# Performance work log

Hardware: AMD Instinct MI355X
Metric: run time of the kernel (lower is better)

## Reference

```python
import jax, jax.numpy as jnp
import numpy as np

N_FFT = 1024
HOP = 256
F_BINS = N_FFT // 2 + 1  # 513


def _make_dft_kernel():
    # torch.hann_window(N) is periodic: 0.5*(1 - cos(2*pi*k/N))
    window = 0.5 * (1.0 - np.cos(2.0 * np.pi * np.arange(N_FFT) / N_FFT))
    # rfft of identity, transposed -> (F, n_fft), then apply window along time axis
    dftm = np.fft.rfft(np.eye(N_FFT)).T * window[None, :]  # complex (F, n_fft)
    # view_as_real + rearrange 'f n ri -> (ri f) n': real block first, imag block second
    kernel = np.concatenate([dftm.real, dftm.imag], axis=0)  # (2F, n_fft)
    return jnp.asarray(kernel, dtype=jnp.float32)


def setup_inputs() -> dict:
    key = jax.random.key(0)
    signal = jax.random.normal(key, (16, 262144), dtype=jnp.float32)
    kernel = _make_dft_kernel()  # (1026, 1024) fixed windowed-DFT matrix (buffer)
    return {"signal": signal, "kernel": kernel}


def reference(signal, kernel):
    # center=True: reflect-pad by n_fft//2 on both sides
    pad = N_FFT // 2
    x = jnp.pad(signal, ((0, 0), (pad, pad)), mode="reflect")  # (B, L)
    B, L = x.shape
    n_frames = (L - N_FFT) // HOP + 1
    # im2col framing: (n_frames, n_fft) gather indices
    idx = jnp.arange(n_frames)[:, None] * HOP + jnp.arange(N_FFT)[None, :]
    frames = x[:, idx]  # (B, n_frames, n_fft)
    # conv1d as GEMM: (B, 2F, n_frames)
    out = jnp.einsum("btn,cn->bct", frames, kernel)
    # rearrange '(ri f) n -> f n ri' with ri outer
    out = out.reshape(B, 2, F_BINS, n_frames)
    return jnp.transpose(out, (0, 2, 3, 1))  # (B, F, n_frames, 2)
```

## Files before the change

### kernel.cpp

```cpp
#include <hip/hip_runtime.h>
#include <hip/hip_bf16.h>
#include <cstdint>


#define HOP 256
#define NFFT 1024
#define FB 513
#define NT 1025
#define NBATCH 16
#define MCH 1026
#define MP2 1280
#define SIGLEN 262144
#define SIGP 263168
#define BM 256
#define BN 128
#define BK 64
#define NKT 16
#define SLOT_BYTES 49152
#define LDS_BYTES (3 * SLOT_BYTES)

typedef __attribute__((ext_vector_type(8))) short short8;
typedef __attribute__((ext_vector_type(4))) float f32x4;
typedef unsigned int u32;

__device__ __forceinline__ unsigned short f2bf(float f) {
  u32 u = __float_as_uint(f);
  u = (u + 0x7FFFu + ((u >> 16) & 1u)) >> 16;
  return (unsigned short)u;
}
__device__ __forceinline__ float bf2f(unsigned short s) {
  return __uint_as_float(((u32)s) << 16);
}

__global__ __launch_bounds__(256) void prep_A(const float* __restrict__ kern,
                                              unsigned short* __restrict__ A) {
  size_t i8 = ((size_t)blockIdx.x * 256 + threadIdx.x) * 8;
  int row = (int)(i8 >> 10);
  int col = (int)(i8 & 1023);
  short8 v = {0, 0, 0, 0, 0, 0, 0, 0};
  if (row < MCH) {
    int f = row >> 1, ri = row & 1;
    int src_row = ri * FB + f;
    const float* s = kern + ((size_t)src_row << 10) + col;
#pragma unroll
    for (int e = 0; e < 8; ++e) v[e] = (short)f2bf(s[e]);
  }
  *(short8*)(A + i8) = v;
}

__global__ __launch_bounds__(256) void prep_S(const float* __restrict__ sig,
                                              unsigned short* __restrict__ S) {
  size_t i8 = ((size_t)blockIdx.x * 256 + threadIdx.x) * 8;
  int b = (int)(i8 / SIGP);
  int i = (int)(i8 - (size_t)b * SIGP);
  const float* sb = sig + (size_t)b * SIGLEN;
  short8 v;
#pragma unroll
  for (int e = 0; e < 8; ++e) {
    int j = i + e - 512;
    j = (j < 0) ? -j : j;
    j = (j >= SIGLEN) ? (2 * SIGLEN - 2 - j) : j;
    v[e] = (short)f2bf(sb[j]);
  }
  *(short8*)(S + i8) = v;
}

__device__ __forceinline__ void async16(void* lds, const void* g) {
  __builtin_amdgcn_global_load_lds(
      (const __attribute__((address_space(1))) u32*)g,
      (__attribute__((address_space(3))) u32*)lds, 16, 0, 0);
}

__global__ __launch_bounds__(512, 2) void stft_mm(const unsigned short* __restrict__ A,
                                                  const unsigned short* __restrict__ S,
                                                  float* __restrict__ out) {
  extern __shared__ char smem[];

  const int tid = threadIdx.x;
  const int lane = tid & 63;
  const int wid = tid >> 6;
  const int wr = wid >> 1;
  const int wc = wid & 1;
  const int lr = lane & 15;
  const int g16 = lane >> 4;

  const int bid = blockIdx.x;
  const int wg = (bid & 7) * 64 + (bid >> 3);
  const int mt = wg & 3;
  const int r2 = wg >> 2;
  const int nt = r2 & 7;
  const int b  = r2 >> 3;

  const int c0 = mt * BM;
  const int t0 = nt * BN;

  const char* Ab = (const char*)A;
  const char* Sb = (const char*)(S + (size_t)b * SIGP);

#define STAGE_TILE(kt, s)                                                      \
  {                                                                            \
    char* As_ = smem + (s) * SLOT_BYTES;                                       \
    char* Bs_ = As_ + 32768;                                                   \
    _Pragma("unroll") for (int j = 0; j < 4; ++j) {                            \
      const int G0 = j * 512 + wid * 64;                                       \
      u32 p = (u32)(G0 + lane) * 16u;                                          \
      u32 q = p ^ (((p >> 7) & 7u) << 4);                                      \
      const char* src = Ab + ((size_t)(c0 + (int)(q >> 7)) << 11)              \
                           + (kt) * 128 + (int)(q & 127u);                     \
      async16(As_ + (size_t)G0 * 16u, src);                                    \
    }                                                                          \
    _Pragma("unroll") for (int j = 0; j < 2; ++j) {                            \
      const int G0 = j * 512 + wid * 64;                                       \
      u32 p = (u32)(G0 + lane) * 16u;                                          \
      u32 q = p ^ (((p >> 7) & 7u) << 4);                                      \
      const char* src = Sb + ((size_t)(t0 + (int)(q >> 7)) << 9)               \
                           + (kt) * 128 + (int)(q & 127u);                     \
      async16(Bs_ + (size_t)G0 * 16u, src);                                    \
    }                                                                          \
  }

  STAGE_TILE(0, 0)
  STAGE_TILE(1, 1)
  asm volatile("s_waitcnt vmcnt(6)" ::: "memory");
  __builtin_amdgcn_s_barrier();
  asm volatile("" ::: "memory");

  u32 qa[4], qb[4];
#pragma unroll
  for (int mi = 0; mi < 4; ++mi) qa[mi] = (u32)((wr * 64 + mi * 16 + lr) * 128 + g16 * 16);
#pragma unroll
  for (int ni = 0; ni < 4; ++ni) qb[ni] = (u32)((wc * 64 + ni * 16 + lr) * 128 + g16 * 16);

  f32x4 acc[4][4] = {};

#pragma unroll
  for (int k = 0; k < NKT; ++k) {
    const char* As = smem + (k % 3) * SLOT_BYTES;
    const char* Bs = As + 32768;
    short8 af[2][4], bfv[2][4];
#pragma unroll
    for (int h = 0; h < 2; ++h) {
#pragma unroll
      for (int mi = 0; mi < 4; ++mi) {
        u32 q = qa[mi] + (u32)(h * 64);
        u32 p = q ^ (((q >> 7) & 7u) << 4);
        af[h][mi] = *(const short8*)(As + p);
      }
#pragma unroll
      for (int ni = 0; ni < 4; ++ni) {
        u32 q = qb[ni] + (u32)(h * 64);
        u32 p = q ^ (((q >> 7) & 7u) << 4);
        bfv[h][ni] = *(const short8*)(Bs + p);
      }
    }
    if (k + 2 < NKT) STAGE_TILE(k + 2, (k + 2) % 3)
#pragma unroll
    for (int h = 0; h < 2; ++h)
#pragma unroll
      for (int mi = 0; mi < 4; ++mi)
#pragma unroll
        for (int ni = 0; ni < 4; ++ni)
          acc[mi][ni] = __builtin_amdgcn_mfma_f32_16x16x32_bf16(
              af[h][mi], bfv[h][ni], acc[mi][ni], 0, 0, 0);
    if (k <= NKT - 3)      asm volatile("s_waitcnt vmcnt(6)" ::: "memory");
    else                   asm volatile("s_waitcnt vmcnt(0)" ::: "memory");
    __builtin_amdgcn_s_barrier();
    asm volatile("" ::: "memory");
  }
#undef STAGE_TILE

#pragma unroll
  for (int mi = 0; mi < 4; ++mi) {
    const int cb = c0 + wr * 64 + mi * 16 + g16 * 4;
    const int f0 = cb >> 1;
#pragma unroll
    for (int ni = 0; ni < 4; ++ni) {
      const int t = t0 + wc * 64 + ni * 16 + lr;
      *(float2*)(out + ((((size_t)b * FB + f0) * NT + t) << 1)) =
          make_float2(acc[mi][ni][0], acc[mi][ni][1]);
      *(float2*)(out + ((((size_t)b * FB + f0 + 1) * NT + t) << 1)) =
          make_float2(acc[mi][ni][2], acc[mi][ni][3]);
    }
  }
}

__global__ __launch_bounds__(256) void stft_edge(const unsigned short* __restrict__ A,
                                                 const unsigned short* __restrict__ S,
                                                 float* __restrict__ out) {
  const int wv = blockIdx.x * 4 + (threadIdx.x >> 6);
  const int lane = threadIdx.x & 63;
  int b, f, t;
  if (wv < NBATCH * NT) {
    b = wv / NT; t = wv - b * NT; f = FB - 1;
  } else {
    int u = wv - NBATCH * NT;
    b = u / FB; f = u - b * FB; t = NT - 1;
  }
  const unsigned short* w  = S + (size_t)b * SIGP + (size_t)t * HOP + lane * 16;
  const unsigned short* r0 = A + ((size_t)(2 * f) << 10) + lane * 16;
  const unsigned short* r1 = r0 + 1024;
  short8 wv0 = *(const short8*)w,  wv1 = *(const short8*)(w + 8);
  short8 a0  = *(const short8*)r0, a1  = *(const short8*)(r0 + 8);
  short8 b0  = *(const short8*)r1, b1  = *(const short8*)(r1 + 8);
  float d0 = 0.f, d1 = 0.f;
#pragma unroll
  for (int e = 0; e < 8; ++e) {
    float x0 = bf2f((unsigned short)wv0[e]), x1 = bf2f((unsigned short)wv1[e]);
    d0 += bf2f((unsigned short)a0[e]) * x0 + bf2f((unsigned short)a1[e]) * x1;
    d1 += bf2f((unsigned short)b0[e]) * x0 + bf2f((unsigned short)b1[e]) * x1;
  }
#pragma unroll
  for (int m = 32; m; m >>= 1) {
    d0 += __shfl_xor(d0, m);
    d1 += __shfl_xor(d1, m);
  }
  if (lane == 0)
    *(float2*)(out + ((((size_t)b * FB + f) * NT + t) << 1)) = make_float2(d0, d1);
}

extern "C" void kernel_launch(void* const* d_in, const int* in_sizes, int n_in,
                              void* d_out, int out_size, void* d_ws, size_t ws_size,
                              hipStream_t stream) {
  const float* sig = (const float*)d_in[0];
  const float* kern = (const float*)d_in[1];
  float* out = (float*)d_out;

  unsigned short* wsA = (unsigned short*)d_ws;
  unsigned short* wsS = wsA + (size_t)MP2 * NFFT;

  (void)hipFuncSetAttribute((const void*)stft_mm,
                            hipFuncAttributeMaxDynamicSharedMemorySize, LDS_BYTES);

  prep_A<<<dim3(MP2 * NFFT / 8 / 256), 256, 0, stream>>>(kern, wsA);
  prep_S<<<dim3(NBATCH * SIGP / 8 / 256), 256, 0, stream>>>(sig, wsS);
  stft_mm<<<dim3(4 * 8 * NBATCH), 512, LDS_BYTES, stream>>>(wsA, wsS, out);
  stft_edge<<<dim3((NBATCH * NT + NBATCH * FB) / 4), 256, 0, stream>>>(wsA, wsS, out);
}
```

Before: 64.97 us.

## Halve K tile to 32 and switch to double-buffered static LDS pipeline

The GEMM K-step drops from 64 to 32 and the three-slot, two-ahead async pipeline becomes a two-slot, one-ahead one held in static shared memory (48KB instead of 144KB). Launch bounds now request 4 blocks per CU instead of 2, and the swizzle is changed to match the 64-byte rows. The intent is higher occupancy and less LDS pressure. In exchange there are twice as many barriers per tile, less prefetch depth, and a full __syncthreads that waits on all outstanding loads. Only 512 blocks are launched, so there may be too few blocks to use the extra occupancy.

```diff
diff --git a/kernel.cpp b/kernel.cpp
--- a/kernel.cpp
+++ b/kernel.cpp
@@ -14,10 +14,11 @@
 #define SIGP 263168
 #define BM 256
 #define BN 128
-#define BK 64
-#define NKT 16
-#define SLOT_BYTES 49152
-#define LDS_BYTES (3 * SLOT_BYTES)
+#define BK 32
+#define NKT 32
+#define A_BYTES 16384
+#define B_BYTES 8192
+#define SLOT_BYTES (A_BYTES + B_BYTES)
 
 typedef __attribute__((ext_vector_type(8))) short short8;
 typedef __attribute__((ext_vector_type(4))) float f32x4;
@@ -71,10 +72,10 @@
       (__attribute__((address_space(3))) u32*)lds, 16, 0, 0);
 }
 
-__global__ __launch_bounds__(512, 2) void stft_mm(const unsigned short* __restrict__ A,
+__global__ __launch_bounds__(512, 4) void stft_mm(const unsigned short* __restrict__ A,
                                                   const unsigned short* __restrict__ S,
                                                   float* __restrict__ out) {
-  extern __shared__ char smem[];
+  __shared__ __align__(16) char smem[2][SLOT_BYTES];
 
   const int tid = threadIdx.x;
   const int lane = tid & 63;
@@ -99,73 +100,64 @@
 
 #define STAGE_TILE(kt, s)                                                      \
   {                                                                            \
-    char* As_ = smem + (s) * SLOT_BYTES;                                       \
-    char* Bs_ = As_ + 32768;                                                   \
-    _Pragma("unroll") for (int j = 0; j < 4; ++j) {                            \
-      const int G0 = j * 512 + wid * 64;                                       \
-      u32 p = (u32)(G0 + lane) * 16u;                                          \
-      u32 q = p ^ (((p >> 7) & 7u) << 4);                                      \
-      const char* src = Ab + ((size_t)(c0 + (int)(q >> 7)) << 11)              \
-                           + (kt) * 128 + (int)(q & 127u);                     \
-      async16(As_ + (size_t)G0 * 16u, src);                                    \
-    }                                                                          \
+    char* As_ = &smem[s][0];                                                   \
+    char* Bs_ = &smem[s][A_BYTES];                                             \
     _Pragma("unroll") for (int j = 0; j < 2; ++j) {                            \
       const int G0 = j * 512 + wid * 64;                                       \
       u32 p = (u32)(G0 + lane) * 16u;                                          \
-      u32 q = p ^ (((p >> 7) & 7u) << 4);                                      \
-      const char* src = Sb + ((size_t)(t0 + (int)(q >> 7)) << 9)               \
-                           + (kt) * 128 + (int)(q & 127u);                     \
+      u32 q = p ^ (((p >> 7) & 3u) << 4);                                      \
+      const char* src = Ab + ((size_t)(c0 + (int)(q >> 6)) << 11)              \
+                           + (kt) * 64 + (int)(q & 63u);                       \
+      async16(As_ + (size_t)G0 * 16u, src);                                    \
+    }                                                                          \
+    {                                                                          \
+      const int G0 = wid * 64;                                                 \
+      u32 p = (u32)(G0 + lane) * 16u;                                          \
+      u32 q = p ^ (((p >> 7) & 3u) << 4);                                      \
+      const char* src = Sb + ((size_t)(t0 + (int)(q >> 6)) << 9)               \
+                           + (kt) * 64 + (int)(q & 63u);                       \
       async16(Bs_ + (size_t)G0 * 16u, src);                                    \
     }                                                                          \
   }
 
   STAGE_TILE(0, 0)
-  STAGE_TILE(1, 1)
-  asm volatile("s_waitcnt vmcnt(6)" ::: "memory");
-  __builtin_amdgcn_s_barrier();
-  asm volatile("" ::: "memory");
-
-  u32 qa[4], qb[4];
-#pragma unroll
-  for (int mi = 0; mi < 4; ++mi) qa[mi] = (u32)((wr * 64 + mi * 16 + lr) * 128 + g16 * 16);
-#pragma unroll
-  for (int ni = 0; ni < 4; ++ni) qb[ni] = (u32)((wc * 64 + ni * 16 + lr) * 128 + g16 * 16);
+  __syncthreads();
+
+  u32 pa[4], pb[4];
+#pragma unroll
+  for (int mi = 0; mi < 4; ++mi) {
+    u32 q = (u32)((wr * 64 + mi * 16 + lr) * 64 + g16 * 16);
+    pa[mi] = q ^ (((q >> 7) & 3u) << 4);
+  }
+#pragma unroll
+  for (int ni = 0; ni < 4; ++ni) {
+    u32 q = (u32)((wc * 64 + ni * 16 + lr) * 64 + g16 * 16);
+    pb[ni] = q ^ (((q >> 7) & 3u) << 4);
+  }
 
   f32x4 acc[4][4] = {};
 
 #pragma unroll
   for (int k = 0; k < NKT; ++k) {
-    const char* As = smem + (k % 3) * SLOT_BYTES;
-    const char* Bs = As + 32768;
-    short8 af[2][4], bfv[2][4];
-#pragma unroll
-    for (int h = 0; h < 2; ++h) {
-#pragma unroll
-      for (int mi = 0; mi < 4; ++mi) {
-        u32 q = qa[mi] + (u32)(h * 64);
-        u32 p = q ^ (((q >> 7) & 7u) << 4);
-        af[h][mi] = *(const short8*)(As + p);
-      }
-#pragma unroll
-      for (int ni = 0; ni < 4; ++ni) {
-        u32 q = qb[ni] + (u32)(h * 64);
-        u32 p = q ^ (((q >> 7) & 7u) << 4);
-        bfv[h][ni] = *(const short8*)(Bs + p);
-      }
-    }
-    if (k + 2 < NKT) STAGE_TILE(k + 2, (k + 2) % 3)
-#pragma unroll
-    for (int h = 0; h < 2; ++h)
-#pragma unroll
-      for (int mi = 0; mi < 4; ++mi)
-#pragma unroll
-        for (int ni = 0; ni < 4; ++ni)
-          acc[mi][ni] = __builtin_amdgcn_mfma_f32_16x16x32_bf16(
-              af[h][mi], bfv[h][ni], acc[mi][ni], 0, 0, 0);
-    if (k <= NKT - 3)      asm volatile("s_waitcnt vmcnt(6)" ::: "memory");
-    else                   asm volatile("s_waitcnt vmcnt(0)" ::: "memory");
-    __builtin_amdgcn_s_barrier();
-    asm volatile("" ::: "memory");
+    const char* As = &smem[k & 1][0];
+    const char* Bs = As + A_BYTES;
+
+    if (k + 1 < NKT) STAGE_TILE(k + 1, (k + 1) & 1)
+
+    short8 af[4], bfv[4];
+#pragma unroll
+    for (int mi = 0; mi < 4; ++mi) af[mi] = *(const short8*)(As + pa[mi]);
+#pragma unroll
+    for (int ni = 0; ni < 4; ++ni) bfv[ni] = *(const short8*)(Bs + pb[ni]);
+
+#pragma unroll
+    for (int mi = 0; mi < 4; ++mi)
+#pragma unroll
+      for (int ni = 0; ni < 4; ++ni)
+        acc[mi][ni] = __builtin_amdgcn_mfma_f32_16x16x32_bf16(
+            af[mi], bfv[ni], acc[mi][ni], 0, 0, 0);
+
+    if (k + 1 < NKT) __syncthreads();
   }
 #undef STAGE_TILE
 
@@ -228,11 +220,8 @@
   unsigned short* wsA = (unsigned short*)d_ws;
   unsigned short* wsS = wsA + (size_t)MP2 * NFFT;
 
-  (void)hipFuncSetAttribute((const void*)stft_mm,
-                            hipFuncAttributeMaxDynamicSharedMemorySize, LDS_BYTES);
-
   prep_A<<<dim3(MP2 * NFFT / 8 / 256), 256, 0, stream>>>(kern, wsA);
   prep_S<<<dim3(NBATCH * SIGP / 8 / 256), 256, 0, stream>>>(sig, wsS);
-  stft_mm<<<dim3(4 * 8 * NBATCH), 512, LDS_BYTES, stream>>>(wsA, wsS, out);
+  stft_mm<<<dim3(4 * 8 * NBATCH), 512, 0, stream>>>(wsA, wsS, out);
   stft_edge<<<dim3((NBATCH * NT + NBATCH * FB) / 4), 256, 0, stream>>>(wsA, wsS, out);
 }
```

Measured after the change: 69.71 us. 7.3% more time.
